# Kernel optimization log

Measured on AMD Instinct MI355X. Metric: run time of the kernel, lower is better.

The kernel has to match this reference:

```python
import jax, jax.numpy as jnp
import numpy as np

N, C, H = 4096, 768, 12
HD = C // H
SCALE = HD ** -0.5


def setup_inputs() -> dict:
    key = jax.random.key(0)
    k1, k2, k3 = jax.random.split(key, 3)
    x = jax.random.normal(k1, (N, C), dtype=jnp.float32)
    w_qkv = jax.random.normal(k2, (C, 3 * C), dtype=jnp.float32) * (C ** -0.5)
    w_proj = jax.random.normal(k3, (C, C), dtype=jnp.float32) * (C ** -0.5)
    b_proj = jnp.zeros((C,), dtype=jnp.float32)
    return {"x": x, "w_qkv": w_qkv, "w_proj": w_proj, "b_proj": b_proj}


def reference(x, w_qkv, w_proj, b_proj):
    n, c = x.shape
    # fused QKV projection (qkv_bias=False): [N, 3C] -> [3, H, N, hd]
    qkv = (x @ w_qkv).reshape(n, 3, H, HD)
    qkv = jnp.transpose(qkv, (1, 2, 0, 3))  # (3, H, N, hd)
    q, k, v = qkv[0], qkv[1], qkv[2]
    # scaled dot-product attention per head: (H, N, N)
    attn = jnp.einsum('hnd,hmd->hnm', q, k) * SCALE
    attn = jax.nn.softmax(attn, axis=-1)
    # attn_drop is identity (rate=0, eval mode)
    out = jnp.einsum('hnm,hmd->hnd', attn, v)          # (H, N, hd)
    out = jnp.transpose(out, (1, 0, 2)).reshape(n, c)  # (N, C)
    # output projection (bias by default in nn.Dense); proj_drop identity
    return out @ w_proj + b_proj
```

## Files before the change

kernel.cpp:

```cpp
#include <hip/hip_runtime.h>

#define N_TOK 4096
#define C_DIM 768
#define H_NUM 12
#define QKV_N 2304

typedef __attribute__((ext_vector_type(8))) short bf16x8;
typedef __attribute__((ext_vector_type(4))) float f32x4;
typedef __attribute__((ext_vector_type(16))) float f32x16;
typedef __attribute__((ext_vector_type(4))) unsigned int u32x4;

static __device__ __forceinline__ unsigned short f2bf(float f) {
  unsigned u = __builtin_bit_cast(unsigned, f);
  u += 0x7FFF + ((u >> 16) & 1);
  return (unsigned short)(u >> 16);
}

static __device__ __forceinline__ float exp2_fast(float x) {
  float r; asm("v_exp_f32 %0, %1" : "=v"(r) : "v"(x)); return r;
}

#define GLOAD_LDS16(g, l)                                                     \
  __builtin_amdgcn_global_load_lds(                                           \
      (const __attribute__((address_space(1))) void*)(g),                     \
      (__attribute__((address_space(3))) void*)(l), 16, 0, 0)

#define Q_SCALE 0.18033688011112042f

__global__ __launch_bounds__(256) void conv_bf16(
    const float* __restrict__ in, unsigned short* __restrict__ out, int n8) {
  const int i = blockIdx.x * 256 + threadIdx.x;
  if (i >= n8) return;
  const float4 a = reinterpret_cast<const float4*>(in)[i * 2];
  const float4 b = reinterpret_cast<const float4*>(in)[i * 2 + 1];
  unsigned short tmp[8] = {f2bf(a.x), f2bf(a.y), f2bf(a.z), f2bf(a.w),
                           f2bf(b.x), f2bf(b.y), f2bf(b.z), f2bf(b.w)};
  reinterpret_cast<bf16x8*>(out)[i] = *reinterpret_cast<bf16x8*>(tmp);
}

__global__ __launch_bounds__(256) void transpose_cvt(
    const float* __restrict__ in, unsigned short* __restrict__ out,
    int K, int N) {
  __shared__ unsigned short T[64][65];
  const int t = threadIdx.x;
  const int k0 = blockIdx.y * 64, n0 = blockIdx.x * 64;
  {
    const int r = t >> 2, qd = t & 3;
#pragma unroll
    for (int i = 0; i < 4; ++i) {
      const int c = qd * 16 + i * 4;
      const float4 v = *reinterpret_cast<const float4*>(
          &in[(size_t)(k0 + r) * N + n0 + c]);
      T[r][c + 0] = f2bf(v.x); T[r][c + 1] = f2bf(v.y);
      T[r][c + 2] = f2bf(v.z); T[r][c + 3] = f2bf(v.w);
    }
  }
  __syncthreads();
#pragma unroll
  for (int i = 0; i < 2; ++i) {
    const int cid = t + i * 256;
    const int rn = cid >> 3, cx = cid & 7;
    unsigned short tmp[8];
#pragma unroll
    for (int j = 0; j < 8; ++j) tmp[j] = T[cx * 8 + j][rn];
    *reinterpret_cast<bf16x8*>(&out[(size_t)(n0 + rn) * K + k0 + cx * 8]) =
        *reinterpret_cast<bf16x8*>(tmp);
  }
}

__global__ __launch_bounds__(256) void gemm_qkv_bf16(
    const unsigned short* __restrict__ A, const unsigned short* __restrict__ Bt,
    unsigned short* __restrict__ qw, unsigned short* __restrict__ kw,
    unsigned short* __restrict__ vw) {
  __shared__ unsigned short As[128 * 32];
  __shared__ unsigned short Bs[128 * 32];
  const int t = threadIdx.x;
  const int lane = t & 63, wid = t >> 6;
  const int lr = lane & 15, lg = lane >> 4;
  const int lid = blockIdx.y * 18 + blockIdx.x;
  const int swz = (lid & 7) * 72 + (lid >> 3);
  const int m_base = (swz / 18) * 128, n_base = (swz % 18) * 128;
  const int wm = (wid >> 1) * 64, wn = (wid & 1) * 64;
  const int c_row = lane >> 2;
  const int c_col = (lane & 3) * 8;

  f32x4 acc[4][4];
#pragma unroll
  for (int mt = 0; mt < 4; ++mt)
#pragma unroll
    for (int nt = 0; nt < 4; ++nt) acc[mt][nt] = (f32x4){0.f, 0.f, 0.f, 0.f};

  for (int kt = 0; kt < 24; ++kt) {
    const int k0 = kt * 32;
    __syncthreads();
#pragma unroll
    for (int i = 0; i < 2; ++i) {
      const int ch = wid * 2 + i;
      GLOAD_LDS16(&A[(size_t)(m_base + ch * 16 + c_row) * 768 + k0 + c_col],
                  &As[ch * 512]);
      GLOAD_LDS16(&Bt[(size_t)(n_base + ch * 16 + c_row) * 768 + k0 + c_col],
                  &Bs[ch * 512]);
    }
    __syncthreads();
    bf16x8 af[4], bfr[4];
#pragma unroll
    for (int mt = 0; mt < 4; ++mt)
      af[mt] = *reinterpret_cast<const bf16x8*>(&As[(wm + mt * 16 + lr) * 32 + lg * 8]);
#pragma unroll
    for (int nt = 0; nt < 4; ++nt)
      bfr[nt] = *reinterpret_cast<const bf16x8*>(&Bs[(wn + nt * 16 + lr) * 32 + lg * 8]);
#pragma unroll
    for (int mt = 0; mt < 4; ++mt)
#pragma unroll
      for (int nt = 0; nt < 4; ++nt)
        acc[mt][nt] = __builtin_amdgcn_mfma_f32_16x16x32_bf16(af[mt], bfr[nt],
                                                              acc[mt][nt], 0, 0, 0);
  }
#pragma unroll
  for (int mt = 0; mt < 4; ++mt)
#pragma unroll
    for (int nt = 0; nt < 4; ++nt)
#pragma unroll
      for (int r = 0; r < 4; ++r) {
        const int m = m_base + wm + mt * 16 + lg * 4 + r;
        const int c = n_base + wn + nt * 16 + lr;
        const float v = acc[mt][nt][r];
        const int which = c / 768;
        const int cc = c - which * 768;
        const int h = cc >> 6, d = cc & 63;
        if (which == 0) {
          qw[((size_t)h * N_TOK + m) * 64 + d] = f2bf(v * Q_SCALE);
        } else if (which == 1) {
          kw[((size_t)h * N_TOK + m) * 64 + d] = f2bf(v);
        } else {
          vw[((size_t)h * 64 + d) * N_TOK + m] = f2bf(v);
        }
      }
}

__global__ __launch_bounds__(256) void gemm_proj_bf16(
    const unsigned short* __restrict__ A, const unsigned short* __restrict__ Bt,
    const float* __restrict__ bias, float* __restrict__ out) {
  __shared__ unsigned short As[128 * 32];
  __shared__ unsigned short Bs[128 * 32];
  const int t = threadIdx.x;
  const int lane = t & 63, wid = t >> 6;
  const int lr = lane & 15, lg = lane >> 4;
  const int lid = blockIdx.y * 6 + blockIdx.x;
  const int swz = (lid & 7) * 24 + (lid >> 3);
  const int m_base = (swz / 6) * 128, n_base = (swz % 6) * 128;
  const int wm = (wid >> 1) * 64, wn = (wid & 1) * 64;
  const int c_row = lane >> 2;
  const int c_col = (lane & 3) * 8;

  f32x4 acc[4][4];
#pragma unroll
  for (int mt = 0; mt < 4; ++mt)
#pragma unroll
    for (int nt = 0; nt < 4; ++nt) acc[mt][nt] = (f32x4){0.f, 0.f, 0.f, 0.f};

  for (int kt = 0; kt < 24; ++kt) {
    const int k0 = kt * 32;
    __syncthreads();
#pragma unroll
    for (int i = 0; i < 2; ++i) {
      const int ch = wid * 2 + i;
      GLOAD_LDS16(&A[(size_t)(m_base + ch * 16 + c_row) * 768 + k0 + c_col],
                  &As[ch * 512]);
      GLOAD_LDS16(&Bt[(size_t)(n_base + ch * 16 + c_row) * 768 + k0 + c_col],
                  &Bs[ch * 512]);
    }
    __syncthreads();
    bf16x8 af[4], bfr[4];
#pragma unroll
    for (int mt = 0; mt < 4; ++mt)
      af[mt] = *reinterpret_cast<const bf16x8*>(&As[(wm + mt * 16 + lr) * 32 + lg * 8]);
#pragma unroll
    for (int nt = 0; nt < 4; ++nt)
      bfr[nt] = *reinterpret_cast<const bf16x8*>(&Bs[(wn + nt * 16 + lr) * 32 + lg * 8]);
#pragma unroll
    for (int mt = 0; mt < 4; ++mt)
#pragma unroll
      for (int nt = 0; nt < 4; ++nt)
        acc[mt][nt] = __builtin_amdgcn_mfma_f32_16x16x32_bf16(af[mt], bfr[nt],
                                                              acc[mt][nt], 0, 0, 0);
  }
#pragma unroll
  for (int nt = 0; nt < 4; ++nt) {
    const int n = n_base + wn + nt * 16 + lr;
    const float bv = bias[n];
#pragma unroll
    for (int mt = 0; mt < 4; ++mt)
#pragma unroll
      for (int r = 0; r < 4; ++r) {
        const int m = m_base + wm + mt * 16 + lg * 4 + r;
        out[(size_t)m * 768 + n] = acc[mt][nt][r] + bv;
      }
  }
}

__global__ __launch_bounds__(256) void attn_kernel(
    const unsigned short* __restrict__ qw, const unsigned short* __restrict__ kw,
    const unsigned short* __restrict__ vw, unsigned short* __restrict__ ow) {
  __shared__ unsigned short smem[18432];
  const int t = threadIdx.x;
  const int lane = t & 63;
  const int wid = t >> 6;
  const int qsub = wid & 1;
  const int kvh = wid >> 1;
  const int q31 = lane & 31;
  const int hi = lane >> 5;
  const int swz = (blockIdx.x & 7) * 96 + (blockIdx.x >> 3);
  const int h = swz >> 6;
  const int qt = swz & 63;
  const int q0 = qt * 64 + qsub * 32;

  unsigned short* Ks = &smem[kvh * 9216];
  unsigned short* Vs = Ks + 4608;

  const unsigned short* kbase = &kw[(size_t)h * N_TOK * 64];
  const unsigned short* vbase = &vw[(size_t)h * 64 * N_TOK];
  const int kv0 = kvh * 2048;

  bf16x8 qf[4];
#pragma unroll
  for (int ks = 0; ks < 4; ++ks)
    qf[ks] = *reinterpret_cast<const bf16x8*>(
        &qw[((size_t)h * N_TOK + q0 + q31) * 64 + ks * 16 + hi * 8]);

  f32x16 acc0, acc1;
#pragma unroll
  for (int r = 0; r < 16; ++r) { acc0[r] = 0.f; acc1[r] = 0.f; }
  float l_run = 0.f;

  const int tg = t & 127;
  const int srow = tg >> 3;
  const int sseg = (tg & 7) * 8;

  bf16x8 kst[4], vst[4];
#pragma unroll
  for (int i = 0; i < 4; ++i) {
    const int row = srow + i * 16;
    kst[i] = *reinterpret_cast<const bf16x8*>(&kbase[(size_t)(kv0 + row) * 64 + sseg]);
    vst[i] = *reinterpret_cast<const bf16x8*>(&vbase[(size_t)row * N_TOK + kv0 + sseg]);
  }

  for (int kvt = 0; kvt < 32; ++kvt) {
    const int kv = kv0 + kvt * 64;
    __syncthreads();
#pragma unroll
    for (int i = 0; i < 4; ++i) {
      const int row = srow + i * 16;
      *reinterpret_cast<bf16x8*>(&Ks[row * 72 + sseg]) = kst[i];
      *reinterpret_cast<bf16x8*>(&Vs[row * 72 + sseg]) = vst[i];
    }
    __syncthreads();
    const int kvn = (kvt + 1 < 32) ? kv + 64 : kv0;
#pragma unroll
    for (int i = 0; i < 4; ++i) {
      const int row = srow + i * 16;
      kst[i] = *reinterpret_cast<const bf16x8*>(&kbase[(size_t)(kvn + row) * 64 + sseg]);
      vst[i] = *reinterpret_cast<const bf16x8*>(&vbase[(size_t)row * N_TOK + kvn + sseg]);
    }

#pragma unroll
    for (int ct = 0; ct < 2; ++ct) {
      f32x16 s;
#pragma unroll
      for (int r = 0; r < 16; ++r) s[r] = 0.f;
      __builtin_amdgcn_s_setprio(1);
#pragma unroll
      for (int ks = 0; ks < 4; ++ks) {
        const bf16x8 kf = *reinterpret_cast<const bf16x8*>(
            &Ks[(ct * 32 + q31) * 72 + ks * 16 + hi * 8]);
        s = __builtin_amdgcn_mfma_f32_32x32x16_bf16(kf, qf[ks], s, 0, 0, 0);
      }
      __builtin_amdgcn_s_setprio(0);

      float p[16];
#pragma unroll
      for (int r = 0; r < 16; ++r) p[r] = exp2_fast(s[r]);
      float s8[8];
#pragma unroll
      for (int r = 0; r < 8; ++r) s8[r] = p[r] + p[r + 8];
#pragma unroll
      for (int r = 0; r < 4; ++r) s8[r] = s8[r] + s8[r + 4];
      l_run += (s8[0] + s8[1]) + (s8[2] + s8[3]);

      unsigned dw[8];
#pragma unroll
      for (int m2 = 0; m2 < 8; ++m2)
        asm("v_cvt_pk_bf16_f32 %0, %1, %2"
            : "=v"(dw[m2]) : "v"(p[2 * m2]), "v"(p[2 * m2 + 1]));
      asm("v_permlane32_swap_b32 %0, %1" : "+v"(dw[0]), "+v"(dw[2]));
      asm("v_permlane32_swap_b32 %0, %1" : "+v"(dw[1]), "+v"(dw[3]));
      asm("v_permlane32_swap_b32 %0, %1" : "+v"(dw[4]), "+v"(dw[6]));
      asm("v_permlane32_swap_b32 %0, %1" : "+v"(dw[5]), "+v"(dw[7]));

      __builtin_amdgcn_s_setprio(1);
#pragma unroll
      for (int ksl = 0; ksl < 2; ++ksl) {
        u32x4 u;
        u.x = dw[ksl * 4 + 0]; u.y = dw[ksl * 4 + 1];
        u.z = dw[ksl * 4 + 2]; u.w = dw[ksl * 4 + 3];
        const bf16x8 pa = __builtin_bit_cast(bf16x8, u);
        const int kg = ct * 2 + ksl;
        const bf16x8 vf0 = *reinterpret_cast<const bf16x8*>(
            &Vs[q31 * 72 + kg * 16 + hi * 8]);
        const bf16x8 vf1 = *reinterpret_cast<const bf16x8*>(
            &Vs[(32 + q31) * 72 + kg * 16 + hi * 8]);
        acc0 = __builtin_amdgcn_mfma_f32_32x32x16_bf16(pa, vf0, acc0, 0, 0, 0);
        acc1 = __builtin_amdgcn_mfma_f32_32x32x16_bf16(pa, vf1, acc1, 0, 0, 0);
      }
      __builtin_amdgcn_s_setprio(0);
    }
  }

  l_run += __shfl_xor(l_run, 32);

  __syncthreads();
  float* ex = reinterpret_cast<float*>(smem) + qsub * 2304;
  if (kvh == 1) {
    float* pdst = ex + lane * 36;
#pragma unroll
    for (int r = 0; r < 16; ++r) { pdst[r] = acc0[r]; pdst[16 + r] = acc1[r]; }
    pdst[32] = l_run;
  }
  __syncthreads();
  if (kvh == 0) {
    const float* psrc = ex + lane * 36;
    const float linv = 1.0f / (l_run + psrc[32]);
#pragma unroll
    for (int r = 0; r < 16; ++r) {
      const int crow = (r & 3) + 8 * (r >> 2) + 4 * hi;
      const float iv = __shfl(linv, crow);
      const size_t base = (size_t)(q0 + crow) * C_DIM + h * 64;
      ow[base + q31] = f2bf((acc0[r] + psrc[r]) * iv);
      ow[base + 32 + q31] = f2bf((acc1[r] + psrc[16 + r]) * iv);
    }
  }
}

extern "C" void kernel_launch(void* const* d_in, const int* in_sizes, int n_in,
                              void* d_out, int out_size, void* d_ws, size_t ws_size,
                              hipStream_t stream) {
  (void)in_sizes; (void)n_in; (void)out_size; (void)ws_size;
  const float* x = (const float*)d_in[0];
  const float* w_qkv = (const float*)d_in[1];
  const float* w_proj = (const float*)d_in[2];
  const float* b_proj = (const float*)d_in[3];
  float* out = (float*)d_out;

  const size_t HNd = (size_t)H_NUM * N_TOK * 64;
  unsigned short* qw = (unsigned short*)d_ws;
  unsigned short* kw = qw + HNd;
  unsigned short* vw = kw + HNd;
  unsigned short* xb = vw + HNd;
  unsigned short* ow = xb;
  unsigned short* wT = xb + HNd;
  unsigned short* wqkvT = wT;
  unsigned short* wprojT = wT;

  conv_bf16<<<dim3((N_TOK * C_DIM / 8 + 255) / 256), 256, 0, stream>>>(
      x, xb, N_TOK * C_DIM / 8);
  transpose_cvt<<<dim3(QKV_N / 64, C_DIM / 64), 256, 0, stream>>>(
      w_qkv, wqkvT, C_DIM, QKV_N);
  gemm_qkv_bf16<<<dim3(QKV_N / 128, N_TOK / 128), 256, 0, stream>>>(
      xb, wqkvT, qw, kw, vw);
  transpose_cvt<<<dim3(C_DIM / 64, C_DIM / 64), 256, 0, stream>>>(
      w_proj, wprojT, C_DIM, C_DIM);
  attn_kernel<<<dim3(768), 256, 0, stream>>>(qw, kw, vw, ow);
  gemm_proj_bf16<<<dim3(C_DIM / 128, N_TOK / 128), 256, 0, stream>>>(
      ow, wprojT, b_proj, out);
}
```

Measured before the change: 147.0 us.

## Split attention KV range across two blocks and merge partial outputs

Each attention block now covers half of the key/value sequence, which doubles the grid from 768 to 1536 blocks and raises GPU occupancy. Each block writes a normalized bf16 partial output plus its softmax denominator. A new merge kernel combines the two halves, weighting each by its denominator. The trade-off is an extra launch, more global traffic for the partials, and a second bf16 rounding of the output. The merge is only valid because no running max is subtracted, so both halves share the same exponent scale.

```diff
diff --git a/kernel.cpp b/kernel.cpp
--- a/kernel.cpp
+++ b/kernel.cpp
@@ -14,6 +14,10 @@
   unsigned u = __builtin_bit_cast(unsigned, f);
   u += 0x7FFF + ((u >> 16) & 1);
   return (unsigned short)(u >> 16);
+}
+
+static __device__ __forceinline__ float bf2f(unsigned short u) {
+  return __builtin_bit_cast(float, (unsigned)u << 16);
 }
 
 static __device__ __forceinline__ float exp2_fast(float x) {
@@ -201,7 +205,8 @@
 
 __global__ __launch_bounds__(256) void attn_kernel(
     const unsigned short* __restrict__ qw, const unsigned short* __restrict__ kw,
-    const unsigned short* __restrict__ vw, unsigned short* __restrict__ ow) {
+    const unsigned short* __restrict__ vw, unsigned short* __restrict__ po0,
+    unsigned short* __restrict__ po1, float* __restrict__ lw) {
   __shared__ unsigned short smem[18432];
   const int t = threadIdx.x;
   const int lane = t & 63;
@@ -210,9 +215,11 @@
   const int kvh = wid >> 1;
   const int q31 = lane & 31;
   const int hi = lane >> 5;
-  const int swz = (blockIdx.x & 7) * 96 + (blockIdx.x >> 3);
-  const int h = swz >> 6;
-  const int qt = swz & 63;
+  const int swz = (blockIdx.x & 7) * 192 + (blockIdx.x >> 3);
+  const int h = swz >> 7;
+  const int rem = swz & 127;
+  const int half = rem >> 6;
+  const int qt = rem & 63;
   const int q0 = qt * 64 + qsub * 32;
 
   unsigned short* Ks = &smem[kvh * 9216];
@@ -220,7 +227,7 @@
 
   const unsigned short* kbase = &kw[(size_t)h * N_TOK * 64];
   const unsigned short* vbase = &vw[(size_t)h * 64 * N_TOK];
-  const int kv0 = kvh * 2048;
+  const int kv0 = half * 2048 + kvh * 1024;
 
   bf16x8 qf[4];
 #pragma unroll
@@ -245,7 +252,7 @@
     vst[i] = *reinterpret_cast<const bf16x8*>(&vbase[(size_t)row * N_TOK + kv0 + sseg]);
   }
 
-  for (int kvt = 0; kvt < 32; ++kvt) {
+  for (int kvt = 0; kvt < 16; ++kvt) {
     const int kv = kv0 + kvt * 64;
     __syncthreads();
 #pragma unroll
@@ -255,7 +262,7 @@
       *reinterpret_cast<bf16x8*>(&Vs[row * 72 + sseg]) = vst[i];
     }
     __syncthreads();
-    const int kvn = (kvt + 1 < 32) ? kv + 64 : kv0;
+    const int kvn = (kvt + 1 < 16) ? kv + 64 : kv0;
 #pragma unroll
     for (int i = 0; i < 4; ++i) {
       const int row = srow + i * 16;
@@ -329,16 +336,41 @@
   __syncthreads();
   if (kvh == 0) {
     const float* psrc = ex + lane * 36;
-    const float linv = 1.0f / (l_run + psrc[32]);
+    const float lt = l_run + psrc[32];
+    const float linv = 1.0f / lt;
+    unsigned short* pout = half ? po1 : po0;
 #pragma unroll
     for (int r = 0; r < 16; ++r) {
       const int crow = (r & 3) + 8 * (r >> 2) + 4 * hi;
       const float iv = __shfl(linv, crow);
       const size_t base = (size_t)(q0 + crow) * C_DIM + h * 64;
-      ow[base + q31] = f2bf((acc0[r] + psrc[r]) * iv);
-      ow[base + 32 + q31] = f2bf((acc1[r] + psrc[16 + r]) * iv);
-    }
-  }
+      pout[base + q31] = f2bf((acc0[r] + psrc[r]) * iv);
+      pout[base + 32 + q31] = f2bf((acc1[r] + psrc[16 + r]) * iv);
+    }
+    if (hi == 0) lw[half * 49152 + h * 4096 + q0 + q31] = lt;
+  }
+}
+
+__global__ __launch_bounds__(256) void attn_merge(
+    unsigned short* __restrict__ po0, const unsigned short* __restrict__ po1,
+    const float* __restrict__ lw) {
+  const int i = blockIdx.x * 256 + threadIdx.x;
+  const int base = i * 8;
+  const int q = base / 768;
+  const int c = base - q * 768;
+  const int h = c >> 6;
+  const float l0 = lw[h * 4096 + q];
+  const float l1 = lw[49152 + h * 4096 + q];
+  const float w = 1.0f / (l0 + l1);
+  const float w0 = l0 * w, w1 = l1 * w;
+  const bf16x8 a = *reinterpret_cast<const bf16x8*>(&po0[base]);
+  const bf16x8 b = *reinterpret_cast<const bf16x8*>(&po1[base]);
+  unsigned short tmp[8];
+#pragma unroll
+  for (int j = 0; j < 8; ++j)
+    tmp[j] = f2bf(w0 * bf2f((unsigned short)a[j]) +
+                  w1 * bf2f((unsigned short)b[j]));
+  *reinterpret_cast<bf16x8*>(&po0[base]) = *reinterpret_cast<bf16x8*>(tmp);
 }
 
 extern "C" void kernel_launch(void* const* d_in, const int* in_sizes, int n_in,
@@ -360,6 +392,8 @@
   unsigned short* wT = xb + HNd;
   unsigned short* wqkvT = wT;
   unsigned short* wprojT = wT;
+  unsigned short* po1 = wT + HNd;
+  float* lw = (float*)(po1 + HNd);
 
   conv_bf16<<<dim3((N_TOK * C_DIM / 8 + 255) / 256), 256, 0, stream>>>(
       x, xb, N_TOK * C_DIM / 8);
@@ -369,7 +403,8 @@
       xb, wqkvT, qw, kw, vw);
   transpose_cvt<<<dim3(C_DIM / 64, C_DIM / 64), 256, 0, stream>>>(
       w_proj, wprojT, C_DIM, C_DIM);
-  attn_kernel<<<dim3(768), 256, 0, stream>>>(qw, kw, vw, ow);
+  attn_kernel<<<dim3(1536), 256, 0, stream>>>(qw, kw, vw, ow, po1, lw);
+  attn_merge<<<dim3(N_TOK * C_DIM / 8 / 256), 256, 0, stream>>>(ow, po1, lw);
   gemm_proj_bf16<<<dim3(C_DIM / 128, N_TOK / 128), 256, 0, stream>>>(
       ow, wprojT, b_proj, out);
 }
```

After: 152.5 us. 1.04x slower.
